# Kernel optimization log

Measured on AMD Instinct MI355X. Metric: run time of the kernel, lower is better.

The kernel has to match this reference:

```python
import jax, jax.numpy as jnp
import numpy as np

HIDDEN_DIM = 2048
NUM_EXPERTS = 64
TOP_K = 8
NUM_TOKENS = 16384


def setup_inputs() -> dict:
    key = jax.random.key(0)
    k_x, k_w, k_b = jax.random.split(key, 3)
    X = jax.random.normal(k_x, (NUM_TOKENS, HIDDEN_DIM), dtype=jnp.float32)
    # nn.Linear(hidden_dim, num_experts): weight [out, in], bias [out]
    bound = 1.0 / np.sqrt(HIDDEN_DIM)
    W_gate = jax.random.uniform(k_w, (NUM_EXPERTS, HIDDEN_DIM), jnp.float32, -bound, bound)
    b_gate = jax.random.uniform(k_b, (NUM_EXPERTS,), jnp.float32, -bound, bound)
    return {"X": X, "W_gate": W_gate, "b_gate": b_gate}


def reference(X, W_gate, b_gate):
    # gate linear: [T, H] @ [H, E] + [E] -> [T, E]
    router_logits = jnp.einsum('th,eh->te', X, W_gate) + b_gate
    # softmax in float32 (matches dtype=torch.float)
    router_probs = jax.nn.softmax(router_logits.astype(jnp.float32), axis=-1)
    # top-k over experts: [T, K]
    router_weights, selected_experts_indices = jax.lax.top_k(router_probs, TOP_K)
    router_weights = router_weights / jnp.sum(router_weights, axis=-1, keepdims=True)
    router_weights = router_weights.astype(X.dtype)
    # one-hot [T, K, E] -> permute(2,1,0) -> [E, K, T]
    expert_mask = jax.nn.one_hot(selected_experts_indices, NUM_EXPERTS, dtype=jnp.int64 if jax.config.jax_enable_x64 else jnp.int32)
    expert_mask = jnp.transpose(expert_mask, (2, 1, 0))
    return (router_logits, router_weights, selected_experts_indices.astype(jnp.int32), expert_mask)
```

## Files before the change

kernel.cpp:

```cpp
#include <hip/hip_runtime.h>

#define NT 16384
#define NH 2048
#define NE 64
#define TOPK 8

#define TB 32
#define KSTEPS 64
#define KQ 4
#define KSW (KSTEPS / KQ)

#define LOFF 0
#define WOFF (NT * NE)
#define IOFF (WOFF + NT * TOPK)
#define MOFF (IOFF + NT * TOPK)

typedef __attribute__((ext_vector_type(8))) short short8;
typedef __attribute__((ext_vector_type(4))) float floatx4;

union FragU { uint4 u; short8 s; };

__device__ __forceinline__ unsigned pack3(float a, float b, unsigned& w1, unsigned& w2) {
    unsigned au = __float_as_uint(a), bu = __float_as_uint(b);
    unsigned ah0 = au & 0xFFFF0000u, bh0 = bu & 0xFFFF0000u;
    float ra = a - __uint_as_float(ah0);
    float rb = b - __uint_as_float(bh0);
    unsigned ar = __float_as_uint(ra), br = __float_as_uint(rb);
    unsigned ah1 = ar & 0xFFFF0000u, bh1 = br & 0xFFFF0000u;
    float sa = ra - __uint_as_float(ah1);
    float sb = rb - __uint_as_float(bh1);
    w1 = bh1 | (ah1 >> 16);
    w2 = (__float_as_uint(sb) & 0xFFFF0000u) | (__float_as_uint(sa) >> 16);
    return bh0 | (ah0 >> 16);
}

__global__ __launch_bounds__(64)
void wconv_kernel(const float* __restrict__ Wg, uint4* __restrict__ wsp) {
    const int b = blockIdx.x;
    const int t = b >> 2, g = b & 3;
    const int l = threadIdx.x;
    const int e  = g * 16 + (l & 15);
    const int k0 = t * 32 + (l >> 4) * 8;
    const float* src = Wg + (size_t)e * NH + k0;
    float4 w0 = *(const float4*)src;
    float4 w1 = *(const float4*)(src + 4);
    unsigned u1[4], u2[4];
    uint4 p0;
    p0.x = pack3(w0.x, w0.y, u1[0], u2[0]);
    p0.y = pack3(w0.z, w0.w, u1[1], u2[1]);
    p0.z = pack3(w1.x, w1.y, u1[2], u2[2]);
    p0.w = pack3(w1.z, w1.w, u1[3], u2[3]);
    uint4* dst = wsp + (size_t)((t * 4 + g) * 3) * 64 + l;
    dst[0]   = p0;
    dst[64]  = make_uint4(u1[0], u1[1], u1[2], u1[3]);
    dst[128] = make_uint4(u2[0], u2[1], u2[2], u2[3]);
}

__global__ __launch_bounds__(512, 4)
void router_kernel(const float* __restrict__ X, const uint4* __restrict__ wsp,
                   const float* __restrict__ bg, float* __restrict__ out) {
    __shared__ __align__(16) float P[KQ][TB][68];
    __shared__ __align__(16) float Ls[TB][68];

    const int tid = threadIdx.x;
    const int w   = tid >> 6;
    const int kh  = w & 3;
    const int th  = w >> 2;
    const int l   = tid & 63;
    const int lr  = l & 15, lq = l >> 4;
    const int tbase = blockIdx.x * TB;

    floatx4 acc[4];
#pragma unroll
    for (int g = 0; g < 4; g++) acc[g] = (floatx4)0.0f;

    const float* xp0 = X + (size_t)(tbase + th * 16 + lr) * NH + kh * (KSW * 32) + lq * 8;
    const uint4* wp = wsp + (size_t)(kh * KSW) * 12 * 64 + l;

    float4 a0lo = *(const float4*)xp0;
    float4 a0hi = *(const float4*)(xp0 + 4);

    {
        float4 z = make_float4(0.f, 0.f, 0.f, 0.f);
#pragma unroll
        for (int m = 0; m < 8; m++) {
            int f2  = tid + 512 * m;
            int seg = f2 >> 3;
            int off = (f2 & 7) << 2;
            *(float4*)(out + MOFF + (size_t)seg * NT + tbase + off) = z;
        }
    }

#pragma unroll 2
    for (int t = 0; t < KSW; t++) {
        FragU b[4][3];
        const uint4* wt = wp + t * 768;
#pragma unroll
        for (int g = 0; g < 4; g++)
#pragma unroll
            for (int p = 0; p < 3; p++)
                b[g][p].u = wt[(g * 3 + p) * 64];

        FragU af[3];
        {
            unsigned u1[4], u2[4];
            uint4 q;
            q.x = pack3(a0lo.x, a0lo.y, u1[0], u2[0]);
            q.y = pack3(a0lo.z, a0lo.w, u1[1], u2[1]);
            q.z = pack3(a0hi.x, a0hi.y, u1[2], u2[2]);
            q.w = pack3(a0hi.z, a0hi.w, u1[3], u2[3]);
            af[0].u = q;
            af[1].u = make_uint4(u1[0], u1[1], u1[2], u1[3]);
            af[2].u = make_uint4(u2[0], u2[1], u2[2], u2[3]);
        }

        if (t + 1 < KSW) {
            const float* nx0 = xp0 + (t + 1) * 32;
            a0lo = *(const float4*)nx0;
            a0hi = *(const float4*)(nx0 + 4);
        }

        __builtin_amdgcn_s_setprio(1);
#pragma unroll
        for (int g = 0; g < 4; g++) {
            acc[g] = __builtin_amdgcn_mfma_f32_16x16x32_bf16(af[0].s, b[g][0].s, acc[g], 0, 0, 0);
            acc[g] = __builtin_amdgcn_mfma_f32_16x16x32_bf16(af[0].s, b[g][1].s, acc[g], 0, 0, 0);
            acc[g] = __builtin_amdgcn_mfma_f32_16x16x32_bf16(af[1].s, b[g][0].s, acc[g], 0, 0, 0);
            acc[g] = __builtin_amdgcn_mfma_f32_16x16x32_bf16(af[1].s, b[g][1].s, acc[g], 0, 0, 0);
            acc[g] = __builtin_amdgcn_mfma_f32_16x16x32_bf16(af[0].s, b[g][2].s, acc[g], 0, 0, 0);
            acc[g] = __builtin_amdgcn_mfma_f32_16x16x32_bf16(af[2].s, b[g][0].s, acc[g], 0, 0, 0);
        }
        __builtin_amdgcn_s_setprio(0);
    }

#pragma unroll
    for (int g = 0; g < 4; g++)
#pragma unroll
        for (int r = 0; r < 4; r++)
            P[kh][th * 16 + lq * 4 + r][g * 16 + lr] = acc[g][r];
    __syncthreads();

    {
        int f4  = tid;
        int tok = f4 >> 4;
        int e4  = (f4 & 15) << 2;
        float4 s0 = *(float4*)&P[0][tok][e4];
        float4 s1 = *(float4*)&P[1][tok][e4];
        float4 s2 = *(float4*)&P[2][tok][e4];
        float4 s3 = *(float4*)&P[3][tok][e4];
        float4 bb = *(const float4*)(bg + e4);
        float4 v;
        v.x = s0.x + s1.x + s2.x + s3.x + bb.x;
        v.y = s0.y + s1.y + s2.y + s3.y + bb.y;
        v.z = s0.z + s1.z + s2.z + s3.z + bb.z;
        v.w = s0.w + s1.w + s2.w + s3.w + bb.w;
        *(float4*)&Ls[tok][e4] = v;
        *(float4*)(out + LOFF + (size_t)tbase * NE + (size_t)f4 * 4) = v;
    }
    __syncthreads();

    if (tid < 256) {
        const int tok = tid >> 3;
        const int el  = tid & 7;
        float4 va = *(float4*)&Ls[tok][el * 8];
        float4 vb = *(float4*)&Ls[tok][el * 8 + 4];
        float v[8] = {va.x, va.y, va.z, va.w, vb.x, vb.y, vb.z, vb.w};

        unsigned msk = 0;
        float m0 = 0.f, ssum = 0.f, myv = 0.f;
        int myi = 0;
#pragma unroll
        for (int r = 0; r < 8; r++) {
            float bv = -3.0e38f; int bi = 64;
#pragma unroll
            for (int j = 0; j < 8; j++) {
                bool better = (((msk >> j) & 1u) == 0u) && (v[j] > bv);
                bv = better ? v[j] : bv;
                bi = better ? (el * 8 + j) : bi;
            }
#pragma unroll
            for (int s2 = 1; s2 < 8; s2 <<= 1) {
                float ov = __shfl_xor(bv, s2);
                int   oi = __shfl_xor(bi, s2);
                bool take = (ov > bv) || (ov == bv && oi < bi);
                bv = take ? ov : bv;
                bi = take ? oi : bi;
            }
            if ((bi >> 3) == el) msk |= (1u << (bi & 7));
            if (r == 0) m0 = bv;
            ssum += __expf(bv - m0);
            if (r == el) { myv = bv; myi = bi; }
        }
        float wgt = __expf(myv - m0) / ssum;
        size_t gt = (size_t)(tbase + tok);
        out[WOFF + gt * TOPK + el] = wgt;
        out[IOFF + gt * TOPK + el] = (float)myi;
        out[MOFF + (size_t)myi * (TOPK * NT) + (size_t)el * NT + gt] = 1.0f;
    }
}

extern "C" void kernel_launch(void* const* d_in, const int* in_sizes, int n_in,
                              void* d_out, int out_size, void* d_ws, size_t ws_size,
                              hipStream_t stream) {
    const float* X  = (const float*)d_in[0];
    const float* Wg = (const float*)d_in[1];
    const float* bg = (const float*)d_in[2];
    float* out = (float*)d_out;
    uint4* wsp = (uint4*)d_ws;

    hipLaunchKernelGGL(wconv_kernel, dim3(KSTEPS * 4), dim3(64), 0, stream, Wg, wsp);
    hipLaunchKernelGGL(router_kernel, dim3(NT / TB), dim3(512), 0, stream,
                       X, (const uint4*)wsp, bg, out);
}
```

Measured before the change: 241.4 us.

## Stage X and weight tiles through LDS with a four-deep async pipeline

The router GEMM now streams X and the pre-split bf16x3 weight fragments into shared memory with global_load_lds over a four-stage ring. It drops the K-split across waves and its partial-sum reduction; waves instead split the expert dimension, with XOR swizzling applied to X rows in LDS. Zeroing of the expert mask moves from the router kernel into the weight-prep kernel. The cost is two barriers per K step and less register-level prefetch, and occupancy changes to 256-thread blocks with a larger LDS footprint.

```diff
diff --git a/kernel.cpp b/kernel.cpp
--- a/kernel.cpp
+++ b/kernel.cpp
@@ -6,9 +6,8 @@
 #define TOPK 8
 
 #define TB 32
-#define KSTEPS 64
-#define KQ 4
-#define KSW (KSTEPS / KQ)
+#define NSTEP 64
+#define DEPTH 4
 
 #define LOFF 0
 #define WOFF (NT * NE)
@@ -19,6 +18,14 @@
 typedef __attribute__((ext_vector_type(4))) float floatx4;
 
 union FragU { uint4 u; short8 s; };
+
+#define WAITVM(n) asm volatile("s_waitcnt vmcnt(" #n ")" ::: "memory")
+
+__device__ __forceinline__ void glds16(const void* g, void* l) {
+    __builtin_amdgcn_global_load_lds(
+        (const __attribute__((address_space(1))) unsigned int*)g,
+        (__attribute__((address_space(3))) unsigned int*)l, 16, 0, 0);
+}
 
 __device__ __forceinline__ unsigned pack3(float a, float b, unsigned& w1, unsigned& w2) {
     unsigned au = __float_as_uint(a), bu = __float_as_uint(b);
@@ -34,169 +41,171 @@
     return bh0 | (ah0 >> 16);
 }
 
-__global__ __launch_bounds__(64)
-void wconv_kernel(const float* __restrict__ Wg, uint4* __restrict__ wsp) {
+__global__ __launch_bounds__(256)
+void prep_kernel(const float* __restrict__ Wg, uint4* __restrict__ wsp,
+                 float* __restrict__ out) {
     const int b = blockIdx.x;
-    const int t = b >> 2, g = b & 3;
-    const int l = threadIdx.x;
-    const int e  = g * 16 + (l & 15);
-    const int k0 = t * 32 + (l >> 4) * 8;
-    const float* src = Wg + (size_t)e * NH + k0;
-    float4 w0 = *(const float4*)src;
-    float4 w1 = *(const float4*)(src + 4);
-    unsigned u1[4], u2[4];
-    uint4 p0;
-    p0.x = pack3(w0.x, w0.y, u1[0], u2[0]);
-    p0.y = pack3(w0.z, w0.w, u1[1], u2[1]);
-    p0.z = pack3(w1.x, w1.y, u1[2], u2[2]);
-    p0.w = pack3(w1.z, w1.w, u1[3], u2[3]);
-    uint4* dst = wsp + (size_t)((t * 4 + g) * 3) * 64 + l;
-    dst[0]   = p0;
-    dst[64]  = make_uint4(u1[0], u1[1], u1[2], u1[3]);
-    dst[128] = make_uint4(u2[0], u2[1], u2[2], u2[3]);
-}
-
-__global__ __launch_bounds__(512, 4)
+    const int tid = threadIdx.x;
+
+    float4 z = make_float4(0.f, 0.f, 0.f, 0.f);
+    float4* mp = (float4*)(out + MOFF) + (size_t)b * 8192 + tid;
+#pragma unroll
+    for (int it = 0; it < 32; it++) mp[it * 256] = z;
+
+    if (tid < 64) {
+        const int t = b >> 2, g = b & 3;
+        const int l = tid;
+        const int e  = g * 16 + (l & 15);
+        const int k0 = t * 32 + (l >> 4) * 8;
+        const float* src = Wg + (size_t)e * NH + k0;
+        float4 w0 = *(const float4*)src;
+        float4 w1 = *(const float4*)(src + 4);
+        unsigned u1[4], u2[4];
+        uint4 p0;
+        p0.x = pack3(w0.x, w0.y, u1[0], u2[0]);
+        p0.y = pack3(w0.z, w0.w, u1[1], u2[1]);
+        p0.z = pack3(w1.x, w1.y, u1[2], u2[2]);
+        p0.w = pack3(w1.z, w1.w, u1[3], u2[3]);
+        uint4* dst = wsp + (size_t)((t * 4 + g) * 3) * 64 + l;
+        dst[0]   = p0;
+        dst[64]  = make_uint4(u1[0], u1[1], u1[2], u1[3]);
+        dst[128] = make_uint4(u2[0], u2[1], u2[2], u2[3]);
+    }
+}
+
+__global__ __launch_bounds__(256, 2)
 void router_kernel(const float* __restrict__ X, const uint4* __restrict__ wsp,
                    const float* __restrict__ bg, float* __restrict__ out) {
-    __shared__ __align__(16) float P[KQ][TB][68];
-    __shared__ __align__(16) float Ls[TB][68];
+    __shared__ uint4 SB[DEPTH][1024];
+    __shared__ float Ls[TB][68];
 
     const int tid = threadIdx.x;
-    const int w   = tid >> 6;
-    const int kh  = w & 3;
-    const int th  = w >> 2;
+    const int wv  = tid >> 6;
     const int l   = tid & 63;
+    const int th  = wv >> 1;
+    const int eh  = wv & 1;
     const int lr  = l & 15, lq = l >> 4;
     const int tbase = blockIdx.x * TB;
 
-    floatx4 acc[4];
-#pragma unroll
-    for (int g = 0; g < 4; g++) acc[g] = (floatx4)0.0f;
-
-    const float* xp0 = X + (size_t)(tbase + th * 16 + lr) * NH + kh * (KSW * 32) + lq * 8;
-    const uint4* wp = wsp + (size_t)(kh * KSW) * 12 * 64 + l;
-
-    float4 a0lo = *(const float4*)xp0;
-    float4 a0hi = *(const float4*)(xp0 + 4);
-
-    {
-        float4 z = make_float4(0.f, 0.f, 0.f, 0.f);
-#pragma unroll
-        for (int m = 0; m < 8; m++) {
-            int f2  = tid + 512 * m;
-            int seg = f2 >> 3;
-            int off = (f2 & 7) << 2;
-            *(float4*)(out + MOFF + (size_t)seg * NT + tbase + off) = z;
-        }
-    }
-
-#pragma unroll 2
-    for (int t = 0; t < KSW; t++) {
-        FragU b[4][3];
-        const uint4* wt = wp + t * 768;
-#pragma unroll
-        for (int g = 0; g < 4; g++)
-#pragma unroll
-            for (int p = 0; p < 3; p++)
-                b[g][p].u = wt[(g * 3 + p) * 64];
-
-        FragU af[3];
-        {
-            unsigned u1[4], u2[4];
-            uint4 q;
-            q.x = pack3(a0lo.x, a0lo.y, u1[0], u2[0]);
-            q.y = pack3(a0lo.z, a0lo.w, u1[1], u2[1]);
-            q.z = pack3(a0hi.x, a0hi.y, u1[2], u2[2]);
-            q.w = pack3(a0hi.z, a0hi.w, u1[3], u2[3]);
-            af[0].u = q;
-            af[1].u = make_uint4(u1[0], u1[1], u1[2], u1[3]);
-            af[2].u = make_uint4(u2[0], u2[1], u2[2], u2[3]);
-        }
-
-        if (t + 1 < KSW) {
-            const float* nx0 = xp0 + (t + 1) * 32;
-            a0lo = *(const float4*)nx0;
-            a0hi = *(const float4*)(nx0 + 4);
-        }
-
-        __builtin_amdgcn_s_setprio(1);
-#pragma unroll
-        for (int g = 0; g < 4; g++) {
-            acc[g] = __builtin_amdgcn_mfma_f32_16x16x32_bf16(af[0].s, b[g][0].s, acc[g], 0, 0, 0);
-            acc[g] = __builtin_amdgcn_mfma_f32_16x16x32_bf16(af[0].s, b[g][1].s, acc[g], 0, 0, 0);
-            acc[g] = __builtin_amdgcn_mfma_f32_16x16x32_bf16(af[1].s, b[g][0].s, acc[g], 0, 0, 0);
-            acc[g] = __builtin_amdgcn_mfma_f32_16x16x32_bf16(af[1].s, b[g][1].s, acc[g], 0, 0, 0);
-            acc[g] = __builtin_amdgcn_mfma_f32_16x16x32_bf16(af[0].s, b[g][2].s, acc[g], 0, 0, 0);
-            acc[g] = __builtin_amdgcn_mfma_f32_16x16x32_bf16(af[2].s, b[g][0].s, acc[g], 0, 0, 0);
-        }
-        __builtin_amdgcn_s_setprio(0);
-    }
-
-#pragma unroll
-    for (int g = 0; g < 4; g++)
-#pragma unroll
-        for (int r = 0; r < 4; r++)
-            P[kh][th * 16 + lq * 4 + r][g * 16 + lr] = acc[g][r];
+    floatx4 acc[2];
+    acc[0] = (floatx4)0.0f;
+    acc[1] = (floatx4)0.0f;
+
+    const int srow = tid >> 3, sg = tid & 7;
+    const float* xsrc0 = X + (size_t)(tbase + srow) * NH + ((sg ^ (srow & 7)) * 4);
+    const uint4* wsrc0 = wsp + (tid & 63);
+
+#define STAGE(t_, s_) do { \
+    glds16(xsrc0 + (t_) * 32, &SB[s_][tid]); \
+    glds16(wsrc0 + ((size_t)(t_) * 12 + (0 * 4 + wv)) * 64, &SB[s_][256 + (0 * 4 + wv) * 64 + l]); \
+    glds16(wsrc0 + ((size_t)(t_) * 12 + (1 * 4 + wv)) * 64, &SB[s_][256 + (1 * 4 + wv) * 64 + l]); \
+    glds16(wsrc0 + ((size_t)(t_) * 12 + (2 * 4 + wv)) * 64, &SB[s_][256 + (2 * 4 + wv) * 64 + l]); \
+} while (0)
+
+#define MFMA6(accv, A0, A1, A2, B0, B1, B2) do { \
+    accv = __builtin_amdgcn_mfma_f32_16x16x32_bf16(A0, B0, accv, 0, 0, 0); \
+    accv = __builtin_amdgcn_mfma_f32_16x16x32_bf16(A0, B1, accv, 0, 0, 0); \
+    accv = __builtin_amdgcn_mfma_f32_16x16x32_bf16(A1, B0, accv, 0, 0, 0); \
+    accv = __builtin_amdgcn_mfma_f32_16x16x32_bf16(A1, B1, accv, 0, 0, 0); \
+    accv = __builtin_amdgcn_mfma_f32_16x16x32_bf16(A0, B2, accv, 0, 0, 0); \
+    accv = __builtin_amdgcn_mfma_f32_16x16x32_bf16(A2, B0, accv, 0, 0, 0); \
+} while (0)
+
+#define CONSUME(s_) do { \
+    const int arow_ = th * 16 + lr; \
+    const float4 lo_ = *(const float4*)&SB[s_][arow_ * 8 + ((2 * lq) ^ (arow_ & 7))]; \
+    const float4 hi_ = *(const float4*)&SB[s_][arow_ * 8 + ((2 * lq + 1) ^ (arow_ & 7))]; \
+    FragU b00, b01, b02, b10, b11, b12; \
+    b00.u = SB[s_][256 + ((eh * 2 + 0) * 3 + 0) * 64 + l]; \
+    b01.u = SB[s_][256 + ((eh * 2 + 0) * 3 + 1) * 64 + l]; \
+    b02.u = SB[s_][256 + ((eh * 2 + 0) * 3 + 2) * 64 + l]; \
+    b10.u = SB[s_][256 + ((eh * 2 + 1) * 3 + 0) * 64 + l]; \
+    b11.u = SB[s_][256 + ((eh * 2 + 1) * 3 + 1) * 64 + l]; \
+    b12.u = SB[s_][256 + ((eh * 2 + 1) * 3 + 2) * 64 + l]; \
+    FragU af0_, af1_, af2_; \
+    { unsigned u1_[4], u2_[4]; uint4 q_; \
+      q_.x = pack3(lo_.x, lo_.y, u1_[0], u2_[0]); \
+      q_.y = pack3(lo_.z, lo_.w, u1_[1], u2_[1]); \
+      q_.z = pack3(hi_.x, hi_.y, u1_[2], u2_[2]); \
+      q_.w = pack3(hi_.z, hi_.w, u1_[3], u2_[3]); \
+      af0_.u = q_; \
+      af1_.u = make_uint4(u1_[0], u1_[1], u1_[2], u1_[3]); \
+      af2_.u = make_uint4(u2_[0], u2_[1], u2_[2], u2_[3]); } \
+    MFMA6(acc[0], af0_.s, af1_.s, af2_.s, b00.s, b01.s, b02.s); \
+    MFMA6(acc[1], af0_.s, af1_.s, af2_.s, b10.s, b11.s, b12.s); \
+} while (0)
+
+    STAGE(0, 0); STAGE(1, 1); STAGE(2, 2); STAGE(3, 3);
+
+#pragma unroll 4
+    for (int t = 0; t < NSTEP - DEPTH; t++) {
+        const int s = t & (DEPTH - 1);
+        WAITVM(12);
+        __builtin_amdgcn_s_barrier();
+        CONSUME(s);
+        asm volatile("s_waitcnt lgkmcnt(0)" ::: "memory");
+        __builtin_amdgcn_s_barrier();
+        STAGE(t + DEPTH, s);
+    }
+    WAITVM(12); __builtin_amdgcn_s_barrier(); CONSUME(0);
+    WAITVM(8);  __builtin_amdgcn_s_barrier(); CONSUME(1);
+    WAITVM(4);  __builtin_amdgcn_s_barrier(); CONSUME(2);
+    WAITVM(0);  __builtin_amdgcn_s_barrier(); CONSUME(3);
+
+    const float bias0 = bg[eh * 32 + lr];
+    const float bias1 = bg[eh * 32 + 16 + lr];
+#pragma unroll
+    for (int rr = 0; rr < 4; rr++) {
+        Ls[th * 16 + lq * 4 + rr][eh * 32 + lr]      = acc[0][rr] + bias0;
+        Ls[th * 16 + lq * 4 + rr][eh * 32 + 16 + lr] = acc[1][rr] + bias1;
+    }
     __syncthreads();
 
-    {
-        int f4  = tid;
+#pragma unroll
+    for (int v = 0; v < 2; v++) {
+        int f4  = v * 256 + tid;
         int tok = f4 >> 4;
         int e4  = (f4 & 15) << 2;
-        float4 s0 = *(float4*)&P[0][tok][e4];
-        float4 s1 = *(float4*)&P[1][tok][e4];
-        float4 s2 = *(float4*)&P[2][tok][e4];
-        float4 s3 = *(float4*)&P[3][tok][e4];
-        float4 bb = *(const float4*)(bg + e4);
-        float4 v;
-        v.x = s0.x + s1.x + s2.x + s3.x + bb.x;
-        v.y = s0.y + s1.y + s2.y + s3.y + bb.y;
-        v.z = s0.z + s1.z + s2.z + s3.z + bb.z;
-        v.w = s0.w + s1.w + s2.w + s3.w + bb.w;
-        *(float4*)&Ls[tok][e4] = v;
-        *(float4*)(out + LOFF + (size_t)tbase * NE + (size_t)f4 * 4) = v;
-    }
-    __syncthreads();
-
-    if (tid < 256) {
-        const int tok = tid >> 3;
-        const int el  = tid & 7;
-        float4 va = *(float4*)&Ls[tok][el * 8];
-        float4 vb = *(float4*)&Ls[tok][el * 8 + 4];
-        float v[8] = {va.x, va.y, va.z, va.w, vb.x, vb.y, vb.z, vb.w};
-
-        unsigned msk = 0;
-        float m0 = 0.f, ssum = 0.f, myv = 0.f;
-        int myi = 0;
-#pragma unroll
-        for (int r = 0; r < 8; r++) {
-            float bv = -3.0e38f; int bi = 64;
-#pragma unroll
-            for (int j = 0; j < 8; j++) {
-                bool better = (((msk >> j) & 1u) == 0u) && (v[j] > bv);
-                bv = better ? v[j] : bv;
-                bi = better ? (el * 8 + j) : bi;
-            }
-#pragma unroll
-            for (int s2 = 1; s2 < 8; s2 <<= 1) {
-                float ov = __shfl_xor(bv, s2);
-                int   oi = __shfl_xor(bi, s2);
-                bool take = (ov > bv) || (ov == bv && oi < bi);
-                bv = take ? ov : bv;
-                bi = take ? oi : bi;
-            }
-            if ((bi >> 3) == el) msk |= (1u << (bi & 7));
-            if (r == 0) m0 = bv;
-            ssum += __expf(bv - m0);
-            if (r == el) { myv = bv; myi = bi; }
+        float4 o = *(const float4*)&Ls[tok][e4];
+        *(float4*)(out + LOFF + (size_t)tbase * NE + (size_t)f4 * 4) = o;
+    }
+
+    const int tok = tid >> 3;
+    const int el  = tid & 7;
+    float4 va = *(const float4*)&Ls[tok][el * 8];
+    float4 vb = *(const float4*)&Ls[tok][el * 8 + 4];
+    float v[8] = {va.x, va.y, va.z, va.w, vb.x, vb.y, vb.z, vb.w};
+
+    unsigned msk = 0;
+    float m0 = 0.f, ssum = 0.f, myv = 0.f;
+    int myi = 0;
+#pragma unroll
+    for (int r = 0; r < 8; r++) {
+        float bv = -3.0e38f; int bi = 64;
+#pragma unroll
+        for (int j = 0; j < 8; j++) {
+            bool better = (((msk >> j) & 1u) == 0u) && (v[j] > bv);
+            bv = better ? v[j] : bv;
+            bi = better ? (el * 8 + j) : bi;
         }
-        float wgt = __expf(myv - m0) / ssum;
-        size_t gt = (size_t)(tbase + tok);
-        out[WOFF + gt * TOPK + el] = wgt;
-        out[IOFF + gt * TOPK + el] = (float)myi;
-        out[MOFF + (size_t)myi * (TOPK * NT) + (size_t)el * NT + gt] = 1.0f;
-    }
+#pragma unroll
+        for (int s2 = 1; s2 < 8; s2 <<= 1) {
+            float ov = __shfl_xor(bv, s2);
+            int   oi = __shfl_xor(bi, s2);
+            bool take = (ov > bv) || (ov == bv && oi < bi);
+            bv = take ? ov : bv;
+            bi = take ? oi : bi;
+        }
+        if ((bi >> 3) == el) msk |= (1u << (bi & 7));
+        if (r == 0) m0 = bv;
+        ssum += __expf(bv - m0);
+        if (r == el) { myv = bv; myi = bi; }
+    }
+    float wgt = __expf(myv - m0) / ssum;
+    size_t gt = (size_t)(tbase + tok);
+    out[WOFF + gt * TOPK + el] = wgt;
+    out[IOFF + gt * TOPK + el] = (float)myi;
+    out[MOFF + (size_t)myi * (TOPK * NT) + (size_t)el * NT + gt] = 1.0f;
 }
 
 extern "C" void kernel_launch(void* const* d_in, const int* in_sizes, int n_in,
@@ -208,7 +217,7 @@
     float* out = (float*)d_out;
     uint4* wsp = (uint4*)d_ws;
 
-    hipLaunchKernelGGL(wconv_kernel, dim3(KSTEPS * 4), dim3(64), 0, stream, Wg, wsp);
-    hipLaunchKernelGGL(router_kernel, dim3(NT / TB), dim3(512), 0, stream,
+    hipLaunchKernelGGL(prep_kernel, dim3(256), dim3(256), 0, stream, Wg, wsp, out);
+    hipLaunchKernelGGL(router_kernel, dim3(NT / TB), dim3(256), 0, stream,
                        X, (const uint4*)wsp, bg, out);
 }
```

New measurement: 232.3 us. -3.8%, faster.
